# Kernel tuning notes

Hardware: AMD Instinct MI355X
Metric: run time of the kernel (lower is better)

## Reference

```python
import jax, jax.numpy as jnp
import numpy as np

B, T, N_EMBD, H, D_HEAD = 4, 2048, 1024, 16, 64

def setup_inputs() -> dict:
    key = jax.random.key(0)
    ks = jax.random.split(key, 6)
    s_in = N_EMBD ** -0.5
    x = jax.random.normal(ks[0], (B, T, N_EMBD), dtype=jnp.float32)
    # per-head Linear(n_embd, d_head, bias=False) weights, stacked: [H, n_embd, d_head]
    Wq = jax.random.normal(ks[1], (H, N_EMBD, D_HEAD), dtype=jnp.float32) * s_in
    Wk = jax.random.normal(ks[2], (H, N_EMBD, D_HEAD), dtype=jnp.float32) * s_in
    Wv = jax.random.normal(ks[3], (H, N_EMBD, D_HEAD), dtype=jnp.float32) * s_in
    # proj: Linear(H*d_head, n_embd) with bias
    Wp = jax.random.normal(ks[4], (H * D_HEAD, N_EMBD), dtype=jnp.float32) * ((H * D_HEAD) ** -0.5)
    bp = jax.random.normal(ks[5], (N_EMBD,), dtype=jnp.float32) * 0.01
    return {"x": x, "Wq": Wq, "Wk": Wk, "Wv": Wv, "Wp": Wp, "bp": bp}

def reference(x, Wq, Wk, Wv, Wp, bp):
    # per-head projections: [B, H, T, d_head]
    q = jnp.einsum('btc,hcd->bhtd', x, Wq)
    k = jnp.einsum('btc,hcd->bhtd', x, Wk)
    v = jnp.einsum('btc,hcd->bhtd', x, Wv)
    scale = q.shape[-1] ** -0.5
    # full (ring-accumulated across P=1 step) non-causal attention
    scores = jnp.einsum('bhtd,bhsd->bhts', q, k) * scale  # [B,H,T,T]
    p = jax.nn.softmax(scores, axis=-1)
    o = jnp.einsum('bhts,bhsd->bhtd', p, v)               # [B,H,T,d]
    o = o.transpose(0, 2, 1, 3).reshape(x.shape[0], x.shape[1], -1)  # [B,T,H*d]
    out = o @ Wp + bp  # output projection (dropout in eval mode = identity)
    return out
```

## Files before the change

### kernel.cpp

```cpp
#include <hip/hip_runtime.h>
#include <hip/hip_bf16.h>

#define T_SEQ 2048
#define NE    1024
#define NH    16
#define DH    64
#define MROWS 8192
#define QKV_N 3072
#define NT    (T_SEQ / 64)

typedef __attribute__((ext_vector_type(8))) short bf16x8;
typedef __attribute__((ext_vector_type(4))) float f32x4;

__device__ __forceinline__ ushort f2b(float f) {
  __hip_bfloat16 h = __float2bfloat16(f);
  return *reinterpret_cast<ushort*>(&h);
}
__device__ __forceinline__ float fast_exp2(float x) {
  float r; asm("v_exp_f32 %0, %1" : "=v"(r) : "v"(x)); return r;
}

__device__ __forceinline__ void gload_lds16(const ushort* g, ushort* l) {
  __builtin_amdgcn_global_load_lds(
      (const __attribute__((address_space(1))) void*)g,
      (__attribute__((address_space(3))) void*)l, 16, 0, 0);
}

__global__ void cvt_x_kernel(const float* __restrict__ x, ushort* __restrict__ xb) {
  int i = blockIdx.x * blockDim.x + threadIdx.x;
  float4 v = reinterpret_cast<const float4*>(x)[i];
  ushort4 o;
  o.x = f2b(v.x); o.y = f2b(v.y); o.z = f2b(v.z); o.w = f2b(v.w);
  reinterpret_cast<ushort4*>(xb)[i] = o;
}

__global__ void wtrans_head(const float* __restrict__ W, ushort* __restrict__ outT, int rowoff) {
  int h = blockIdx.y;
  int c0 = blockIdx.x * 64;
  __shared__ float t[64][65];
  int a = threadIdx.x & 63, i0 = (threadIdx.x >> 6) * 16;
  const float* base = W + (size_t)h * NE * DH;
#pragma unroll
  for (int j = 0; j < 16; ++j)
    t[i0 + j][a] = base[(size_t)(c0 + i0 + j) * DH + a];
  __syncthreads();
#pragma unroll
  for (int j = 0; j < 16; ++j) {
    int d = i0 + j;
    outT[(size_t)(rowoff + h * DH + d) * NE + c0 + a] = f2b(t[a][d]);
  }
}

__global__ void wtrans_sq(const float* __restrict__ W, ushort* __restrict__ outT) {
  int k0 = blockIdx.x * 64, n0 = blockIdx.y * 64;
  __shared__ float t[64][65];
  int a = threadIdx.x & 63, i0 = (threadIdx.x >> 6) * 16;
#pragma unroll
  for (int j = 0; j < 16; ++j)
    t[i0 + j][a] = W[(size_t)(k0 + i0 + j) * NE + n0 + a];
  __syncthreads();
#pragma unroll
  for (int j = 0; j < 16; ++j) {
    int n = i0 + j;
    outT[(size_t)(n0 + n) * NE + k0 + a] = f2b(t[a][n]);
  }
}

template <int OUTF32>
__global__ __launch_bounds__(256, 2) void gemm_bt(
    const ushort* __restrict__ A, const ushort* __restrict__ Bt,
    void* __restrict__ Cout, const float* __restrict__ bias,
    int M, int N, int K) {
  __shared__ alignas(16) ushort Als[128 * 32];
  __shared__ alignas(16) ushort Bls[128 * 32];
  const int tid = threadIdx.x;
  const int lane = tid & 63, w = tid >> 6;
  const int wr = w >> 1, wc = w & 1;
  const int c = lane & 15, g = lane >> 4;
  const int arow0 = blockIdx.x * 128, brow0 = blockIdx.y * 128;
  const int srow = lane >> 2, scol = (lane & 3) * 8;

  f32x4 acc[4][4];
  f32x4 zero = {0.f, 0.f, 0.f, 0.f};
#pragma unroll
  for (int i = 0; i < 4; ++i)
#pragma unroll
    for (int j = 0; j < 4; ++j) acc[i][j] = zero;

  for (int k0 = 0; k0 < K; k0 += 32) {
#pragma unroll
    for (int cc = 0; cc < 2; ++cc) {
      int ch = w * 2 + cc;
      const ushort* ga = A + (size_t)(arow0 + ch * 16 + srow) * K + k0 + scol;
      gload_lds16(ga, &Als[ch * 512]);
      const ushort* gb = Bt + (size_t)(brow0 + ch * 16 + srow) * K + k0 + scol;
      gload_lds16(gb, &Bls[ch * 512]);
    }
    __syncthreads();

    bf16x8 af[4], bfr[4];
#pragma unroll
    for (int t4 = 0; t4 < 4; ++t4) {
      af[t4]  = *(const bf16x8*)&Als[(wr * 64 + t4 * 16 + c) * 32 + g * 8];
      bfr[t4] = *(const bf16x8*)&Bls[(wc * 64 + t4 * 16 + c) * 32 + g * 8];
    }
#pragma unroll
    for (int i = 0; i < 4; ++i)
#pragma unroll
      for (int j = 0; j < 4; ++j)
        acc[i][j] = __builtin_amdgcn_mfma_f32_16x16x32_bf16(af[i], bfr[j], acc[i][j], 0, 0, 0);
    __syncthreads();
  }

#pragma unroll
  for (int i = 0; i < 4; ++i)
#pragma unroll
    for (int j = 0; j < 4; ++j)
#pragma unroll
      for (int r = 0; r < 4; ++r) {
        int row = arow0 + wr * 64 + i * 16 + g * 4 + r;
        int col = brow0 + wc * 64 + j * 16 + c;
        float v = acc[i][j][r];
        if constexpr (OUTF32) {
          ((float*)Cout)[(size_t)row * N + col] = v + bias[col];
        } else {
          ((ushort*)Cout)[(size_t)row * N + col] = f2b(v);
        }
      }
}

__global__ __launch_bounds__(256, 4) void attn_kern(
    const ushort* __restrict__ qkv, ushort* __restrict__ obuf) {
  const int flat = blockIdx.x;
  const int logical = (flat & 7) * 256 + (flat >> 3);
  const int qt = logical & 31, bh = logical >> 5;
  const int b = bh >> 4, h = bh & 15;
  const int lane = threadIdx.x & 63, w = threadIdx.x >> 6;
  const int c = lane & 15, g = lane >> 4;
  const size_t row0 = (size_t)b * T_SEQ;
  const int qc = h * 64, kc = 1024 + h * 64, vc = 2048 + h * 64;
  const int tid = threadIdx.x;

  __shared__ alignas(16) ushort Kls[2][64 * 64];
  __shared__ alignas(16) ushort Vt[2][64 * 64];
  __shared__ alignas(16) ushort Pls[4][16 * 64];

  const float SCL = 0.125f * 1.44269504f;
  bf16x8 aq[2];
  {
    const size_t qrow = row0 + qt * 64 + w * 16 + c;
    aq[0] = *(const bf16x8*)&qkv[qrow * QKV_N + qc + g * 8];
    aq[1] = *(const bf16x8*)&qkv[qrow * QKV_N + qc + 32 + g * 8];
  }

  const int kq0 = (w * 2 + 0) * 64 + lane;
  const int kq1 = (w * 2 + 1) * 64 + lane;
  const int kj0 = kq0 >> 3, kcc0 = ((kq0 & 7) ^ (kj0 & 7)) * 8;
  const int kj1 = kq1 >> 3, kcc1 = ((kq1 & 7) ^ (kj1 & 7)) * 8;
  const int vd0 = (tid & 31) * 2, vs0 = (tid >> 5) * 8;

  float l_part[4] = {0.f, 0.f, 0.f, 0.f};
  f32x4 zero = {0.f, 0.f, 0.f, 0.f};
  f32x4 oacc[4];
#pragma unroll
  for (int dt = 0; dt < 4; ++dt) oacc[dt] = zero;

  {
    gload_lds16(&qkv[(row0 + kj0) * QKV_N + kc + kcc0], &Kls[0][(w * 2 + 0) * 512]);
    gload_lds16(&qkv[(row0 + kj1) * QKV_N + kc + kcc1], &Kls[0][(w * 2 + 1) * 512]);
    uint vr[8];
#pragma unroll
    for (int i = 0; i < 8; ++i)
      vr[i] = *(const uint*)&qkv[(row0 + vs0 + i) * QKV_N + vc + vd0];
    bf16x8 lo, hi;
#pragma unroll
    for (int i = 0; i < 8; ++i) { lo[i] = (short)(vr[i] & 0xffff); hi[i] = (short)(vr[i] >> 16); }
    *(bf16x8*)&Vt[0][(vd0 * 64 + vs0) ^ ((vd0 & 7) << 3)] = lo;
    *(bf16x8*)&Vt[0][((vd0 + 1) * 64 + vs0) ^ (((vd0 + 1) & 7) << 3)] = hi;
  }
  __syncthreads();

  int cur = 0;
  for (int tile = 0; tile < NT; ++tile) {
    const int nb = cur ^ 1;
    bf16x8 vlo, vhi;
    if (tile + 1 < NT) {
      const size_t kv = (size_t)(tile + 1) * 64;
      gload_lds16(&qkv[(row0 + kv + kj0) * QKV_N + kc + kcc0], &Kls[nb][(w * 2 + 0) * 512]);
      gload_lds16(&qkv[(row0 + kv + kj1) * QKV_N + kc + kcc1], &Kls[nb][(w * 2 + 1) * 512]);
      uint vr[8];
#pragma unroll
      for (int i = 0; i < 8; ++i)
        vr[i] = *(const uint*)&qkv[(row0 + kv + vs0 + i) * QKV_N + vc + vd0];
#pragma unroll
      for (int i = 0; i < 8; ++i) { vlo[i] = (short)(vr[i] & 0xffff); vhi[i] = (short)(vr[i] >> 16); }
    }

    f32x4 sa[4];
#pragma unroll
    for (int jt = 0; jt < 4; ++jt) sa[jt] = zero;
#pragma unroll
    for (int ks = 0; ks < 2; ++ks)
#pragma unroll
      for (int jt = 0; jt < 4; ++jt) {
        int j = jt * 16 + c;
        bf16x8 bk = *(const bf16x8*)&Kls[cur][(j * 64 + ks * 32 + g * 8) ^ ((j & 7) << 3)];
        sa[jt] = __builtin_amdgcn_mfma_f32_16x16x32_bf16(aq[ks], bk, sa[jt], 0, 0, 0);
      }

    float pp[4][4];
#pragma unroll
    for (int jt = 0; jt < 4; ++jt)
#pragma unroll
      for (int r = 0; r < 4; ++r) pp[jt][r] = fast_exp2(sa[jt][r] * SCL);
#pragma unroll
    for (int r = 0; r < 4; ++r)
      l_part[r] += (pp[0][r] + pp[1][r]) + (pp[2][r] + pp[3][r]);

#pragma unroll
    for (int jt = 0; jt < 4; ++jt)
#pragma unroll
      for (int r = 0; r < 4; ++r) {
        int i = g * 4 + r, s = jt * 16 + c;
        Pls[w][(i * 64 + s) ^ ((i & 7) << 3)] = f2b(pp[jt][r]);
      }

#pragma unroll
    for (int ks = 0; ks < 2; ++ks) {
      bf16x8 ap = *(const bf16x8*)&Pls[w][(c * 64 + ks * 32 + g * 8) ^ ((c & 7) << 3)];
#pragma unroll
      for (int dt = 0; dt < 4; ++dt) {
        int d = dt * 16 + c;
        bf16x8 bv = *(const bf16x8*)&Vt[cur][(d * 64 + ks * 32 + g * 8) ^ ((d & 7) << 3)];
        oacc[dt] = __builtin_amdgcn_mfma_f32_16x16x32_bf16(ap, bv, oacc[dt], 0, 0, 0);
      }
    }

    if (tile + 1 < NT) {
      *(bf16x8*)&Vt[nb][(vd0 * 64 + vs0) ^ ((vd0 & 7) << 3)] = vlo;
      *(bf16x8*)&Vt[nb][((vd0 + 1) * 64 + vs0) ^ (((vd0 + 1) & 7) << 3)] = vhi;
    }
    __syncthreads();
    cur ^= 1;
  }

#pragma unroll
  for (int r = 0; r < 4; ++r) {
    float L = l_part[r];
#pragma unroll
    for (int mask = 1; mask < 16; mask <<= 1) L += __shfl_xor(L, mask);
    float rinv = 1.0f / L;
#pragma unroll
    for (int dt = 0; dt < 4; ++dt) {
      int R = qt * 64 + w * 16 + g * 4 + r;
      int d = dt * 16 + c;
      obuf[(row0 + R) * (size_t)NE + h * 64 + d] = f2b(oacc[dt][r] * rinv);
    }
  }
}

extern "C" void kernel_launch(void* const* d_in, const int* in_sizes, int n_in,
                              void* d_out, int out_size, void* d_ws, size_t ws_size,
                              hipStream_t stream) {
  const float* x  = (const float*)d_in[0];
  const float* Wq = (const float*)d_in[1];
  const float* Wk = (const float*)d_in[2];
  const float* Wv = (const float*)d_in[3];
  const float* Wp = (const float*)d_in[4];
  const float* bp = (const float*)d_in[5];
  float* out = (float*)d_out;

  char* ws = (char*)d_ws;
  ushort* xb    = (ushort*)(ws + 0);
  ushort* WcatT = (ushort*)(ws + 16777216);
  ushort* WpT   = (ushort*)(ws + 23068672);
  ushort* qkv   = (ushort*)(ws + 25165824);
  ushort* obuf  = (ushort*)(ws + 75497472);

  cvt_x_kernel<<<dim3(8192), dim3(256), 0, stream>>>(x, xb);
  wtrans_head<<<dim3(16, 16), dim3(256), 0, stream>>>(Wq, WcatT, 0);
  wtrans_head<<<dim3(16, 16), dim3(256), 0, stream>>>(Wk, WcatT, 1024);
  wtrans_head<<<dim3(16, 16), dim3(256), 0, stream>>>(Wv, WcatT, 2048);
  wtrans_sq<<<dim3(16, 16), dim3(256), 0, stream>>>(Wp, WpT);

  gemm_bt<0><<<dim3(MROWS / 128, QKV_N / 128), dim3(256), 0, stream>>>(
      xb, WcatT, (void*)qkv, nullptr, MROWS, QKV_N, NE);

  attn_kern<<<dim3(2048), dim3(256), 0, stream>>>(qkv, obuf);

  gemm_bt<1><<<dim3(MROWS / 128, NE / 128), dim3(256), 0, stream>>>(
      obuf, WpT, (void*)out, bp, MROWS, NE, NE);
}
```

Before: 313.5 us.

## Process two 16-row query blocks per wave in attention to reuse K/V tiles

```diff
diff --git a/kernel.cpp b/kernel.cpp
--- a/kernel.cpp
+++ b/kernel.cpp
@@ -129,11 +129,11 @@
       }
 }
 
-__global__ __launch_bounds__(256, 4) void attn_kern(
+__global__ __launch_bounds__(256, 3) void attn_kern(
     const ushort* __restrict__ qkv, ushort* __restrict__ obuf) {
   const int flat = blockIdx.x;
-  const int logical = (flat & 7) * 256 + (flat >> 3);
-  const int qt = logical & 31, bh = logical >> 5;
+  const int logical = (flat & 7) * 128 + (flat >> 3);
+  const int qt = logical & 15, bh = logical >> 4;
   const int b = bh >> 4, h = bh & 15;
   const int lane = threadIdx.x & 63, w = threadIdx.x >> 6;
   const int c = lane & 15, g = lane >> 4;
@@ -143,14 +143,17 @@
 
   __shared__ alignas(16) ushort Kls[2][64 * 64];
   __shared__ alignas(16) ushort Vt[2][64 * 64];
-  __shared__ alignas(16) ushort Pls[4][16 * 64];
+  __shared__ alignas(16) ushort Pls[4][2 * 16 * 64];
 
   const float SCL = 0.125f * 1.44269504f;
-  bf16x8 aq[2];
+  bf16x8 aq0[2], aq1[2];
   {
-    const size_t qrow = row0 + qt * 64 + w * 16 + c;
-    aq[0] = *(const bf16x8*)&qkv[qrow * QKV_N + qc + g * 8];
-    aq[1] = *(const bf16x8*)&qkv[qrow * QKV_N + qc + 32 + g * 8];
+    const size_t q0 = row0 + qt * 128 + w * 32 + c;
+    const size_t q1 = q0 + 16;
+    aq0[0] = *(const bf16x8*)&qkv[q0 * QKV_N + qc + g * 8];
+    aq0[1] = *(const bf16x8*)&qkv[q0 * QKV_N + qc + 32 + g * 8];
+    aq1[0] = *(const bf16x8*)&qkv[q1 * QKV_N + qc + g * 8];
+    aq1[1] = *(const bf16x8*)&qkv[q1 * QKV_N + qc + 32 + g * 8];
   }
 
   const int kq0 = (w * 2 + 0) * 64 + lane;
@@ -159,11 +162,13 @@
   const int kj1 = kq1 >> 3, kcc1 = ((kq1 & 7) ^ (kj1 & 7)) * 8;
   const int vd0 = (tid & 31) * 2, vs0 = (tid >> 5) * 8;
 
-  float l_part[4] = {0.f, 0.f, 0.f, 0.f};
+  float l0 = 0.f, l1 = 0.f;
   f32x4 zero = {0.f, 0.f, 0.f, 0.f};
-  f32x4 oacc[4];
-#pragma unroll
-  for (int dt = 0; dt < 4; ++dt) oacc[dt] = zero;
+  f32x4 oacc0[4], oacc1[4];
+#pragma unroll
+  for (int dt = 0; dt < 4; ++dt) { oacc0[dt] = zero; oacc1[dt] = zero; }
+
+  ushort* Pw = &Pls[w][0];
 
   {
     gload_lds16(&qkv[(row0 + kj0) * QKV_N + kc + kcc0], &Kls[0][(w * 2 + 0) * 512]);
@@ -196,43 +201,52 @@
       for (int i = 0; i < 8; ++i) { vlo[i] = (short)(vr[i] & 0xffff); vhi[i] = (short)(vr[i] >> 16); }
     }
 
-    f32x4 sa[4];
-#pragma unroll
-    for (int jt = 0; jt < 4; ++jt) sa[jt] = zero;
+    f32x4 sa0[4], sa1[4];
+#pragma unroll
+    for (int jt = 0; jt < 4; ++jt) { sa0[jt] = zero; sa1[jt] = zero; }
 #pragma unroll
     for (int ks = 0; ks < 2; ++ks)
 #pragma unroll
       for (int jt = 0; jt < 4; ++jt) {
         int j = jt * 16 + c;
         bf16x8 bk = *(const bf16x8*)&Kls[cur][(j * 64 + ks * 32 + g * 8) ^ ((j & 7) << 3)];
-        sa[jt] = __builtin_amdgcn_mfma_f32_16x16x32_bf16(aq[ks], bk, sa[jt], 0, 0, 0);
-      }
-
-    float pp[4][4];
+        sa0[jt] = __builtin_amdgcn_mfma_f32_16x16x32_bf16(bk, aq0[ks], sa0[jt], 0, 0, 0);
+        sa1[jt] = __builtin_amdgcn_mfma_f32_16x16x32_bf16(bk, aq1[ks], sa1[jt], 0, 0, 0);
+      }
+
 #pragma unroll
     for (int jt = 0; jt < 4; ++jt)
 #pragma unroll
-      for (int r = 0; r < 4; ++r) pp[jt][r] = fast_exp2(sa[jt][r] * SCL);
-#pragma unroll
-    for (int r = 0; r < 4; ++r)
-      l_part[r] += (pp[0][r] + pp[1][r]) + (pp[2][r] + pp[3][r]);
-
+      for (int r = 0; r < 4; ++r) {
+        sa0[jt][r] = fast_exp2(sa0[jt][r] * SCL);
+        sa1[jt][r] = fast_exp2(sa1[jt][r] * SCL);
+      }
+#pragma unroll
+    for (int jt = 0; jt < 4; ++jt) {
+      l0 += (sa0[jt][0] + sa0[jt][1]) + (sa0[jt][2] + sa0[jt][3]);
+      l1 += (sa1[jt][0] + sa1[jt][1]) + (sa1[jt][2] + sa1[jt][3]);
+    }
 #pragma unroll
     for (int jt = 0; jt < 4; ++jt)
 #pragma unroll
-      for (int r = 0; r < 4; ++r) {
-        int i = g * 4 + r, s = jt * 16 + c;
-        Pls[w][(i * 64 + s) ^ ((i & 7) << 3)] = f2b(pp[jt][r]);
+      for (int pr = 0; pr < 2; ++pr) {
+        int col = jt * 16 + g * 4 + 2 * pr;
+        uint u0 = (uint)f2b(sa0[jt][2 * pr]) | ((uint)f2b(sa0[jt][2 * pr + 1]) << 16);
+        uint u1 = (uint)f2b(sa1[jt][2 * pr]) | ((uint)f2b(sa1[jt][2 * pr + 1]) << 16);
+        *(uint*)&Pw[(c * 64 + col) ^ ((c & 7) << 3)] = u0;
+        *(uint*)&Pw[1024 + ((c * 64 + col) ^ ((c & 7) << 3))] = u1;
       }
 
 #pragma unroll
     for (int ks = 0; ks < 2; ++ks) {
-      bf16x8 ap = *(const bf16x8*)&Pls[w][(c * 64 + ks * 32 + g * 8) ^ ((c & 7) << 3)];
+      bf16x8 ap0 = *(const bf16x8*)&Pw[(c * 64 + ks * 32 + g * 8) ^ ((c & 7) << 3)];
+      bf16x8 ap1 = *(const bf16x8*)&Pw[1024 + ((c * 64 + ks * 32 + g * 8) ^ ((c & 7) << 3))];
 #pragma unroll
       for (int dt = 0; dt < 4; ++dt) {
         int d = dt * 16 + c;
         bf16x8 bv = *(const bf16x8*)&Vt[cur][(d * 64 + ks * 32 + g * 8) ^ ((d & 7) << 3)];
-        oacc[dt] = __builtin_amdgcn_mfma_f32_16x16x32_bf16(ap, bv, oacc[dt], 0, 0, 0);
+        oacc0[dt] = __builtin_amdgcn_mfma_f32_16x16x32_bf16(ap0, bv, oacc0[dt], 0, 0, 0);
+        oacc1[dt] = __builtin_amdgcn_mfma_f32_16x16x32_bf16(ap1, bv, oacc1[dt], 0, 0, 0);
       }
     }
 
@@ -244,17 +258,20 @@
     cur ^= 1;
   }
 
+  l0 += __shfl_xor(l0, 16); l0 += __shfl_xor(l0, 32);
+  l1 += __shfl_xor(l1, 16); l1 += __shfl_xor(l1, 32);
 #pragma unroll
   for (int r = 0; r < 4; ++r) {
-    float L = l_part[r];
-#pragma unroll
-    for (int mask = 1; mask < 16; mask <<= 1) L += __shfl_xor(L, mask);
-    float rinv = 1.0f / L;
+    int src = g * 4 + r;
+    float L0 = __shfl(l0, src);
+    float L1 = __shfl(l1, src);
+    float i0 = 1.0f / L0, i1 = 1.0f / L1;
+    int Rbase = qt * 128 + w * 32;
 #pragma unroll
     for (int dt = 0; dt < 4; ++dt) {
-      int R = qt * 64 + w * 16 + g * 4 + r;
-      int d = dt * 16 + c;
-      obuf[(row0 + R) * (size_t)NE + h * 64 + d] = f2b(oacc[dt][r] * rinv);
+      int d = h * 64 + dt * 16 + c;
+      obuf[(row0 + Rbase + 0  + g * 4 + r) * (size_t)NE + d] = f2b(oacc0[dt][r] * i0);
+      obuf[(row0 + Rbase + 16 + g * 4 + r) * (size_t)NE + d] = f2b(oacc1[dt][r] * i1);
     }
   }
 }
@@ -286,7 +303,7 @@
   gemm_bt<0><<<dim3(MROWS / 128, QKV_N / 128), dim3(256), 0, stream>>>(
       xb, WcatT, (void*)qkv, nullptr, MROWS, QKV_N, NE);
 
-  attn_kern<<<dim3(2048), dim3(256), 0, stream>>>(qkv, obuf);
+  attn_kern<<<dim3(1024), dim3(256), 0, stream>>>(qkv, obuf);
 
   gemm_bt<1><<<dim3(MROWS / 128, NE / 128), dim3(256), 0, stream>>>(
       obuf, WpT, (void*)out, bp, MROWS, NE, NE);
```

Result: faster. 296.6 us (-5.4%).
